# Performance work log

Measured on AMD Instinct MI355X. Metric: run time of the kernel, lower is better.

The kernel has to match this reference:

```python
import jax, jax.numpy as jnp
import numpy as np


def setup_inputs() -> dict:
    key = jax.random.key(0)
    ks = jax.random.split(key, 6)
    B, T, E, H, K = 4, 2048, 1024, 16, 3
    x = jax.random.normal(ks[0], (B, T, E), dtype=jnp.float32)
    mem_k = jax.random.normal(ks[1], (B, T, K, E), dtype=jnp.float32)
    mem_v = jax.random.normal(ks[2], (B, T, K, E), dtype=jnp.float32)
    W_attn = jax.random.normal(ks[3], (E, 3 * E), dtype=jnp.float32) * 0.02
    W_proj = jax.random.normal(ks[4], (E, E), dtype=jnp.float32) * 0.02
    gate_bias = jax.random.normal(ks[5], (H, 1, 1), dtype=jnp.float32)
    return {"x": x, "mem_k": mem_k, "mem_v": mem_v, "W_attn": W_attn,
            "W_proj": W_proj, "gate_bias": gate_bias}


def reference(x, mem_k, mem_v, W_attn, W_proj, gate_bias):
    B, T, E = x.shape
    H = gate_bias.shape[0]
    D = E // H
    K = mem_k.shape[2]
    # qkv projection (no bias)
    qkv = x @ W_attn                                   # [B,T,3E]
    q, k, v = jnp.split(qkv, 3, axis=-1)
    q = q.reshape(B, T, H, D).transpose(0, 2, 1, 3)    # [B,H,T,D]
    k = k.reshape(B, T, H, D).transpose(0, 2, 1, 3)
    v = v.reshape(B, T, H, D).transpose(0, 2, 1, 3)
    # causal SDPA (torch default scale = 1/sqrt(head_dim))
    scores = jnp.einsum('bhqd,bhkd->bhqk', q, k) / jnp.sqrt(jnp.asarray(D, q.dtype))
    causal = jnp.tril(jnp.ones((T, T), dtype=bool))
    scores = jnp.where(causal, scores, jnp.finfo(scores.dtype).min)
    attn = jax.nn.softmax(scores, axis=-1)
    y = jnp.einsum('bhqk,bhkd->bhqd', attn, v)         # [B,H,T,D]
    # top-k retrieved memory attention (k small, here 3)
    mk = mem_k.reshape(B, T, K, H, D).transpose(0, 3, 1, 2, 4)  # [B,H,T,K,D]
    mv = mem_v.reshape(B, T, K, H, D).transpose(0, 3, 1, 2, 4)
    # faithful to source: scale = n_embd / n_head**(-0.5) = E*sqrt(H)
    mem_scale = jnp.asarray(E, q.dtype) * jnp.sqrt(jnp.asarray(H, q.dtype))
    mem_qk = jnp.einsum('bhtd,bhtkd->bhtk', q, mk) * mem_scale
    mem_qk = jax.nn.softmax(mem_qk, axis=-1)
    mem_qkv = jnp.einsum('bhtk,bhtkd->bhtd', mem_qk, mv)  # [B,H,T,D]
    # gated fusion, gate_bias broadcasts [H,1,1] over [B,H,T,D]
    combined = mem_qkv * gate_bias + y * (1.0 - gate_bias)
    combined = combined.transpose(0, 2, 1, 3).reshape(B, T, E)
    out = combined @ W_proj
    return out
```

## Files before the change

kernel.cpp:

```cpp
#include <hip/hip_runtime.h>
#include <math.h>

#define Bsz 4
#define Tseq 2048
#define Ed 1024
#define Hh 16
#define E3 (3*Ed)
#define MROWS (Bsz*Tseq)

typedef short short8 __attribute__((ext_vector_type(8)));
typedef _Float16 half8 __attribute__((ext_vector_type(8)));
typedef float floatx4 __attribute__((ext_vector_type(4)));

__device__ __forceinline__ unsigned short f2bf(float f) {
  unsigned int u = __builtin_bit_cast(unsigned int, f);
  u += 0x7fffu + ((u >> 16) & 1u);
  return (unsigned short)(u >> 16);
}
__device__ __forceinline__ float bf2f(unsigned short u) {
  return __builtin_bit_cast(float, ((unsigned int)u) << 16);
}
__device__ __forceinline__ unsigned short f2h(float f) {
  _Float16 h = (_Float16)f;
  return __builtin_bit_cast(unsigned short, h);
}
__device__ __forceinline__ float h2f(unsigned short u) {
  return (float)__builtin_bit_cast(_Float16, u);
}
__device__ __forceinline__ int swz(int row, int col) {
  return row * 64 + ((((col >> 3) ^ (row & 7)) << 3) | (col & 7));
}
__device__ __forceinline__ void gload_lds16(const void* g, void* l) {
  __builtin_amdgcn_global_load_lds(
      (const __attribute__((address_space(1))) void*)g,
      (__attribute__((address_space(3))) void*)l, 16, 0, 0);
}

__global__ __launch_bounds__(256)
void cast_split_k(const float* __restrict__ s, unsigned short* __restrict__ bb,
                  unsigned short* __restrict__ hh, unsigned short* __restrict__ ll,
                  int n4) {
  int i = blockIdx.x * 256 + threadIdx.x;
  if (i >= n4) return;
  float4 v = ((const float4*)s)[i];
  float vv[4] = {v.x, v.y, v.z, v.w};
  unsigned short ob[4], oh[4], ol[4];
  #pragma unroll
  for (int j = 0; j < 4; ++j) {
    ob[j] = f2bf(vv[j]);
    unsigned short h = f2h(vv[j]);
    oh[j] = h;
    ol[j] = f2h(vv[j] - h2f(h));
  }
  ((uint2*)bb)[i] = *(uint2*)ob;
  ((uint2*)hh)[i] = *(uint2*)oh;
  ((uint2*)ll)[i] = *(uint2*)ol;
}

__global__ __launch_bounds__(256)
void transpose_cast(const float* __restrict__ src, int ld, int c0,
                    unsigned short* __restrict__ dst, int Krows) {
  __shared__ float t[64][65];
  const int kb = blockIdx.y * 64, nb = blockIdx.x * 64;
  const int tid = threadIdx.x;
  #pragma unroll
  for (int i = 0; i < 4; ++i) {
    int u = tid + i * 256;
    int r = u >> 4, c4 = u & 15;
    float4 v = *(const float4*)(src + (size_t)(kb + r) * ld + c0 + nb + c4 * 4);
    t[r][c4*4+0] = v.x; t[r][c4*4+1] = v.y; t[r][c4*4+2] = v.z; t[r][c4*4+3] = v.w;
  }
  __syncthreads();
  #pragma unroll
  for (int i = 0; i < 2; ++i) {
    int u = tid + i * 256;
    int rn = u >> 3, g = u & 7;
    unsigned short o[8];
    #pragma unroll
    for (int j = 0; j < 8; ++j) o[j] = f2bf(t[g*8+j][rn]);
    *(uint4*)(dst + (size_t)(nb + rn) * Krows + kb + g * 8) = *(uint4*)o;
  }
}

__global__ __launch_bounds__(256)
void transpose_split(const float* __restrict__ src, int ld, int c0,
                     unsigned short* __restrict__ dh, unsigned short* __restrict__ dl,
                     int Krows) {
  __shared__ float t[64][65];
  const int kb = blockIdx.y * 64, nb = blockIdx.x * 64;
  const int tid = threadIdx.x;
  #pragma unroll
  for (int i = 0; i < 4; ++i) {
    int u = tid + i * 256;
    int r = u >> 4, c4 = u & 15;
    float4 v = *(const float4*)(src + (size_t)(kb + r) * ld + c0 + nb + c4 * 4);
    t[r][c4*4+0] = v.x; t[r][c4*4+1] = v.y; t[r][c4*4+2] = v.z; t[r][c4*4+3] = v.w;
  }
  __syncthreads();
  #pragma unroll
  for (int i = 0; i < 2; ++i) {
    int u = tid + i * 256;
    int rn = u >> 3, g = u & 7;
    unsigned short oh[8], ol[8];
    #pragma unroll
    for (int j = 0; j < 8; ++j) {
      float f = t[g*8+j][rn];
      unsigned short h = f2h(f);
      oh[j] = h;
      ol[j] = f2h(f - h2f(h));
    }
    size_t off = (size_t)(nb + rn) * Krows + kb + g * 8;
    *(uint4*)(dh + off) = *(uint4*)oh;
    *(uint4*)(dl + off) = *(uint4*)ol;
  }
}

template<int N, int KD, bool OBF>
__global__ __launch_bounds__(256)
void gemm_bf16(const unsigned short* __restrict__ A,
               const unsigned short* __restrict__ Bt,
               void* __restrict__ C) {
  __shared__ __align__(16) unsigned short As[128 * 64];
  __shared__ __align__(16) unsigned short Bs[128 * 64];
  const int tid = threadIdx.x;
  const int w = tid >> 6, L = tid & 63, Ln = L & 15, Lq = L >> 4;
  const int wm = w & 1, wn = w >> 1;
  const int m0 = blockIdx.y * 128, n0 = blockIdx.x * 128;
  const int lr = L >> 3, lc = (L & 7) * 8;

  floatx4 acc[4][4];
  #pragma unroll
  for (int mt = 0; mt < 4; ++mt)
    #pragma unroll
    for (int nt = 0; nt < 4; ++nt) acc[mt][nt] = (floatx4)0.f;

  for (int kt = 0; kt < KD; kt += 64) {
    #pragma unroll
    for (int c = 0; c < 4; ++c) {
      int r0 = w * 32 + c * 8;
      gload_lds16(A  + (size_t)(m0 + r0 + lr) * KD + kt + lc, &As[r0 * 64]);
      gload_lds16(Bt + (size_t)(n0 + r0 + lr) * KD + kt + lc, &Bs[r0 * 64]);
    }
    __syncthreads();
    #pragma unroll
    for (int kc = 0; kc < 2; ++kc) {
      short8 af[4], bfr[4];
      #pragma unroll
      for (int mt = 0; mt < 4; ++mt)
        af[mt] = *(const short8*)&As[(wm*64 + mt*16 + Ln) * 64 + kc*32 + Lq*8];
      #pragma unroll
      for (int nt = 0; nt < 4; ++nt)
        bfr[nt] = *(const short8*)&Bs[(wn*64 + nt*16 + Ln) * 64 + kc*32 + Lq*8];
      #pragma unroll
      for (int mt = 0; mt < 4; ++mt)
        #pragma unroll
        for (int nt = 0; nt < 4; ++nt)
          acc[mt][nt] = __builtin_amdgcn_mfma_f32_16x16x32_bf16(af[mt], bfr[nt], acc[mt][nt], 0, 0, 0);
    }
    __syncthreads();
  }
  #pragma unroll
  for (int mt = 0; mt < 4; ++mt)
    #pragma unroll
    for (int nt = 0; nt < 4; ++nt)
      #pragma unroll
      for (int r = 0; r < 4; ++r) {
        size_t row = m0 + wm*64 + mt*16 + Lq*4 + r;
        int col = n0 + wn*64 + nt*16 + Ln;
        if (OBF) ((unsigned short*)C)[row * N + col] = f2bf(acc[mt][nt][r]);
        else     ((float*)C)[row * N + col] = acc[mt][nt][r];
      }
}

template<int N, int KD>
__global__ __launch_bounds__(256)
void gemm_f16x3(const unsigned short* __restrict__ Ah,
                const unsigned short* __restrict__ Al,
                const unsigned short* __restrict__ Bh,
                const unsigned short* __restrict__ Bl,
                float* __restrict__ C) {
  __shared__ __align__(16) unsigned short Ash[128 * 32];
  __shared__ __align__(16) unsigned short Asl[128 * 32];
  __shared__ __align__(16) unsigned short Bsh[128 * 32];
  __shared__ __align__(16) unsigned short Bsl[128 * 32];
  const int tid = threadIdx.x;
  const int w = tid >> 6, L = tid & 63, Ln = L & 15, Lq = L >> 4;
  const int wm = w & 1, wn = w >> 1;
  const int m0 = blockIdx.y * 128, n0 = blockIdx.x * 128;
  const int lr = L >> 2, lc = (L & 3) * 8;

  floatx4 acc[4][4];
  #pragma unroll
  for (int mt = 0; mt < 4; ++mt)
    #pragma unroll
    for (int nt = 0; nt < 4; ++nt) acc[mt][nt] = (floatx4)0.f;

  for (int kt = 0; kt < KD; kt += 32) {
    #pragma unroll
    for (int c = 0; c < 2; ++c) {
      int r0 = w * 32 + c * 16;
      size_t offA = (size_t)(m0 + r0 + lr) * KD + kt + lc;
      size_t offB = (size_t)(n0 + r0 + lr) * KD + kt + lc;
      gload_lds16(Ah + offA, &Ash[r0 * 32]);
      gload_lds16(Al + offA, &Asl[r0 * 32]);
      gload_lds16(Bh + offB, &Bsh[r0 * 32]);
      gload_lds16(Bl + offB, &Bsl[r0 * 32]);
    }
    __syncthreads();
    half8 afh[4], afl[4], bfh[4], bfl[4];
    #pragma unroll
    for (int mt = 0; mt < 4; ++mt) {
      afh[mt] = *(const half8*)&Ash[(wm*64 + mt*16 + Ln) * 32 + Lq*8];
      afl[mt] = *(const half8*)&Asl[(wm*64 + mt*16 + Ln) * 32 + Lq*8];
    }
    #pragma unroll
    for (int nt = 0; nt < 4; ++nt) {
      bfh[nt] = *(const half8*)&Bsh[(wn*64 + nt*16 + Ln) * 32 + Lq*8];
      bfl[nt] = *(const half8*)&Bsl[(wn*64 + nt*16 + Ln) * 32 + Lq*8];
    }
    #pragma unroll
    for (int mt = 0; mt < 4; ++mt)
      #pragma unroll
      for (int nt = 0; nt < 4; ++nt) {
        acc[mt][nt] = __builtin_amdgcn_mfma_f32_16x16x32_f16(afh[mt], bfh[nt], acc[mt][nt], 0, 0, 0);
        acc[mt][nt] = __builtin_amdgcn_mfma_f32_16x16x32_f16(afh[mt], bfl[nt], acc[mt][nt], 0, 0, 0);
        acc[mt][nt] = __builtin_amdgcn_mfma_f32_16x16x32_f16(afl[mt], bfh[nt], acc[mt][nt], 0, 0, 0);
      }
    __syncthreads();
  }
  #pragma unroll
  for (int mt = 0; mt < 4; ++mt)
    #pragma unroll
    for (int nt = 0; nt < 4; ++nt)
      #pragma unroll
      for (int r = 0; r < 4; ++r) {
        size_t row = m0 + wm*64 + mt*16 + Lq*4 + r;
        int col = n0 + wn*64 + nt*16 + Ln;
        C[row * N + col] = acc[mt][nt][r];
      }
}

__global__ __launch_bounds__(512, 4)
void flash_mfma(const float* __restrict__ qf, const unsigned short* __restrict__ kv,
                unsigned short* __restrict__ y) {
  __shared__ __align__(16) unsigned short Ks[2][64 * 64];
  __shared__ __align__(16) unsigned short Vt[2][64 * 64];
  __shared__ __align__(16) unsigned short Ps[8][16 * 64];
  const int ib = blockIdx.x;
  const int bh = blockIdx.y;
  const int b = bh >> 4, h = bh & 15;
  const int tid = threadIdx.x;
  const int w = tid >> 6, L = tid & 63;
  const int Ln = L & 15, Lq = L >> 4;
  const size_t base = (size_t)b * Tseq;
  const int hof = h * 64;

  for (int t = 0; t < 2; ++t) {
    const int qt = t ? ib : 15 - ib;
    const int q0 = qt * 128;
    const int nkt = 2 * qt + 2;

    short8 qfr[2];
    {
      const float* qp = qf + (base + q0 + w*16 + Ln) * Ed + hof;
      #pragma unroll
      for (int kc = 0; kc < 2; ++kc) {
        float v[8];
        *(float4*)&v[0] = *(const float4*)(qp + kc*32 + Lq*8);
        *(float4*)&v[4] = *(const float4*)(qp + kc*32 + Lq*8 + 4);
        short8 tt;
        #pragma unroll
        for (int j = 0; j < 8; ++j) tt[j] = (short)f2bf(v[j]);
        qfr[kc] = tt;
      }
    }

    float m_i[4], l_i[4];
    floatx4 O[4];
    #pragma unroll
    for (int r = 0; r < 4; ++r) { m_i[r] = -3.0e38f; l_i[r] = 0.f; }
    #pragma unroll
    for (int nt = 0; nt < 4; ++nt) O[nt] = (floatx4)0.f;

    {
      int c = tid >> 3, g = tid & 7;
      const unsigned short* kvp = kv + (base + c) * 2048 + hof + g * 8;
      uint4 k4 = *(const uint4*)kvp;
      *(uint4*)&Ks[0][c*64 + ((g ^ (c & 7)) << 3)] = k4;
      unsigned short vv[8];
      *(uint4*)vv = *(const uint4*)(kvp + 1024);
      #pragma unroll
      for (int j = 0; j < 8; ++j) Vt[0][swz(g*8 + j, c)] = vv[j];
    }
    __syncthreads();

    int cur = 0;
    for (int kt = 0; kt < nkt; ++kt) {
      uint4 kreg, vreg;
      const bool pre = (kt + 1 < nkt);
      const int c = tid >> 3, g = tid & 7;
      if (pre) {
        const unsigned short* kvp = kv + (base + (kt+1)*64 + c) * 2048 + hof + g * 8;
        kreg = *(const uint4*)kvp;
        vreg = *(const uint4*)(kvp + 1024);
      }

      short8 kb[4][2];
      #pragma unroll
      for (int nt = 0; nt < 4; ++nt) {
        int krow = nt*16 + Ln;
        #pragma unroll
        for (int kc = 0; kc < 2; ++kc)
          kb[nt][kc] = *(const short8*)&Ks[cur][krow*64 + ((((kc*4 + Lq) ^ (krow & 7)) << 3))];
      }
      floatx4 S[4];
      #pragma unroll
      for (int nt = 0; nt < 4; ++nt) {
        floatx4 a = (floatx4)0.f;
        a = __builtin_amdgcn_mfma_f32_16x16x32_bf16(qfr[0], kb[nt][0], a, 0, 0, 0);
        a = __builtin_amdgcn_mfma_f32_16x16x32_bf16(qfr[1], kb[nt][1], a, 0, 0, 0);
        S[nt] = a;
      }
      #pragma unroll
      for (int nt = 0; nt < 4; ++nt)
        #pragma unroll
        for (int r = 0; r < 4; ++r) S[nt][r] *= 0.125f;
      if (kt >= 2*qt) {
        int rowg = q0 + w*16 + Lq*4;
        #pragma unroll
        for (int nt = 0; nt < 4; ++nt) {
          int colg = kt*64 + nt*16 + Ln;
          #pragma unroll
          for (int r = 0; r < 4; ++r)
            if (colg > rowg + r) S[nt][r] = -3.0e38f;
        }
      }

      #pragma unroll
      for (int r = 0; r < 4; ++r) {
        float mx = fmaxf(fmaxf(S[0][r], S[1][r]), fmaxf(S[2][r], S[3][r]));
        mx = fmaxf(mx, __shfl_xor(mx, 1));
        mx = fmaxf(mx, __shfl_xor(mx, 2));
        mx = fmaxf(mx, __shfl_xor(mx, 4));
        mx = fmaxf(mx, __shfl_xor(mx, 8));
        float mnew = fmaxf(m_i[r], mx);
        float alpha = __expf(m_i[r] - mnew);
        m_i[r] = mnew;
        float rs = 0.f;
        #pragma unroll
        for (int nt = 0; nt < 4; ++nt) {
          float p = __expf(S[nt][r] - mnew);
          S[nt][r] = p;
          rs += p;
        }
        rs += __shfl_xor(rs, 1);
        rs += __shfl_xor(rs, 2);
        rs += __shfl_xor(rs, 4);
        rs += __shfl_xor(rs, 8);
        l_i[r] = l_i[r] * alpha + rs;
        #pragma unroll
        for (int nt = 0; nt < 4; ++nt) O[nt][r] *= alpha;
        int prow = Lq*4 + r;
        #pragma unroll
        for (int nt = 0; nt < 4; ++nt)
          Ps[w][swz(prow, nt*16 + Ln)] = f2bf(S[nt][r]);
      }

      short8 vb[4][2], pf[2];
      #pragma unroll
      for (int nt = 0; nt < 4; ++nt) {
        int vrow = nt*16 + Ln;
        #pragma unroll
        for (int kc = 0; kc < 2; ++kc)
          vb[nt][kc] = *(const short8*)&Vt[cur][vrow*64 + ((((kc*4 + Lq) ^ (vrow & 7)) << 3))];
      }
      {
        int prow = Ln;
        #pragma unroll
        for (int kc = 0; kc < 2; ++kc)
          pf[kc] = *(const short8*)&Ps[w][prow*64 + ((((kc*4 + Lq) ^ (prow & 7)) << 3))];
      }
      #pragma unroll
      for (int nt = 0; nt < 4; ++nt) {
        O[nt] = __builtin_amdgcn_mfma_f32_16x16x32_bf16(pf[0], vb[nt][0], O[nt], 0, 0, 0);
        O[nt] = __builtin_amdgcn_mfma_f32_16x16x32_bf16(pf[1], vb[nt][1], O[nt], 0, 0, 0);
      }

      if (pre) {
        *(uint4*)&Ks[cur^1][c*64 + ((g ^ (c & 7)) << 3)] = kreg;
        unsigned short vv[8];
        *(uint4*)vv = vreg;
        #pragma unroll
        for (int j = 0; j < 8; ++j) Vt[cur^1][swz(g*8 + j, c)] = vv[j];
      }
      __syncthreads();
      cur ^= 1;
    }

    #pragma unroll
    for (int r = 0; r < 4; ++r) {
      float inv = 1.f / l_i[r];
      size_t rb = (base + q0 + w*16 + Lq*4 + r) * Ed + hof;
      #pragma unroll
      for (int nt = 0; nt < 4; ++nt)
        y[rb + nt*16 + Ln] = f2bf(O[nt][r] * inv);
    }
  }
}

__global__ __launch_bounds__(256)
void mem_gate(const float* __restrict__ qf, const float* __restrict__ mem_k,
              const float* __restrict__ mem_v, const float* __restrict__ gate,
              unsigned short* __restrict__ y) {
  const int tid = threadIdx.x;
  const int lane = tid & 63;
  const int g = (blockIdx.x << 2) | (tid >> 6);
  const int h = g & 15;
  const int bt = g >> 4;
  const float q = qf[(size_t)bt * Ed + h*64 + lane];
  const size_t mb = ((size_t)bt * 3) * Ed + h*64 + lane;

  float s[3];
  #pragma unroll
  for (int k = 0; k < 3; ++k) {
    float p = q * mem_k[mb + (size_t)k * Ed];
    p += __shfl_xor(p, 1);  p += __shfl_xor(p, 2);  p += __shfl_xor(p, 4);
    p += __shfl_xor(p, 8);  p += __shfl_xor(p, 16); p += __shfl_xor(p, 32);
    s[k] = p * 4096.0f;
  }
  float mx = fmaxf(s[0], fmaxf(s[1], s[2]));
  float w0 = __expf(s[0] - mx), w1 = __expf(s[1] - mx), w2 = __expf(s[2] - mx);
  float inv = 1.f / (w0 + w1 + w2);
  float ov = (w0 * mem_v[mb] + w1 * mem_v[mb + Ed] + w2 * mem_v[mb + 2*Ed]) * inv;
  float gb = gate[h];
  unsigned short* yp = y + (size_t)bt * Ed + h*64 + lane;
  float yv = bf2f(*yp);
  *yp = f2bf(ov * gb + yv * (1.f - gb));
}

extern "C" void kernel_launch(void* const* d_in, const int* in_sizes, int n_in,
                              void* d_out, int out_size, void* d_ws, size_t ws_size,
                              hipStream_t stream) {
  const float* x      = (const float*)d_in[0];
  const float* mem_k  = (const float*)d_in[1];
  const float* mem_v  = (const float*)d_in[2];
  const float* W_attn = (const float*)d_in[3];
  const float* W_proj = (const float*)d_in[4];
  const float* gate   = (const float*)d_in[5];
  float* out = (float*)d_out;

  float* qf32          = (float*)d_ws;
  unsigned short* kvb  = (unsigned short*)(qf32 + (size_t)MROWS*Ed);
  unsigned short* ybf  = kvb + (size_t)MROWS*2048;
  unsigned short* xb   = ybf + (size_t)MROWS*Ed;
  unsigned short* wkv  = xb  + (size_t)MROWS*Ed;
  unsigned short* wp   = wkv + (size_t)2048*Ed;
  unsigned short* xh  = (unsigned short*)d_out;
  unsigned short* xl  = xh + (size_t)MROWS*Ed;
  unsigned short* wqh = kvb;
  unsigned short* wql = wqh + (size_t)Ed*Ed;

  cast_split_k<<<(MROWS*Ed/4 + 255)/256, 256, 0, stream>>>(x, xb, xh, xl, MROWS*Ed/4);
  transpose_split<<<dim3(Ed/64, Ed/64), 256, 0, stream>>>(W_attn, E3, 0, wqh, wql, Ed);
  transpose_cast<<<dim3(2048/64, Ed/64), 256, 0, stream>>>(W_attn, E3, Ed, wkv, Ed);
  transpose_cast<<<dim3(Ed/64, Ed/64), 256, 0, stream>>>(W_proj, Ed, 0, wp, Ed);
  gemm_f16x3<Ed, Ed>
      <<<dim3(Ed/128, MROWS/128), 256, 0, stream>>>(xh, xl, wqh, wql, qf32);
  gemm_bf16<2048, Ed, true>
      <<<dim3(2048/128, MROWS/128), 256, 0, stream>>>(xb, wkv, kvb);
  flash_mfma<<<dim3(8, Bsz*Hh), 512, 0, stream>>>(qf32, kvb, ybf);
  mem_gate<<<(MROWS*Hh)/4, 256, 0, stream>>>(qf32, mem_k, mem_v, gate, ybf);
  gemm_bf16<Ed, Ed, false>
      <<<dim3(Ed/128, MROWS/128), 256, 0, stream>>>(ybf, wp, out);
}
```

Baseline: 530.5 us.

## Fuse memory-gate into flash epilogue and deepen f16x3 GEMM K-tile

Removes the separate mem_gate kernel and computes the top-k memory attention and gated blend inside the flash attention epilogue. This avoids re-reading and re-writing the bf16 y buffer and saves one launch. The split-f16 GEMM now stages 64-wide K tiles per barrier instead of 32, which halves the number of sync rounds at the cost of doubled LDS use. The flash grid is also reordered so that heads vary fastest across blocks. The epilogue's memory loads are strided per lane and could underuse bandwidth compared with the old kernel's contiguous per-wave reads.

Result: slower. 559.8 us (+5.5%).

```diff
diff --git a/kernel.cpp b/kernel.cpp
--- a/kernel.cpp
+++ b/kernel.cpp
@@ -179,15 +179,15 @@
                 const unsigned short* __restrict__ Bh,
                 const unsigned short* __restrict__ Bl,
                 float* __restrict__ C) {
-  __shared__ __align__(16) unsigned short Ash[128 * 32];
-  __shared__ __align__(16) unsigned short Asl[128 * 32];
-  __shared__ __align__(16) unsigned short Bsh[128 * 32];
-  __shared__ __align__(16) unsigned short Bsl[128 * 32];
+  __shared__ __align__(16) unsigned short Ash[128 * 64];
+  __shared__ __align__(16) unsigned short Asl[128 * 64];
+  __shared__ __align__(16) unsigned short Bsh[128 * 64];
+  __shared__ __align__(16) unsigned short Bsl[128 * 64];
   const int tid = threadIdx.x;
   const int w = tid >> 6, L = tid & 63, Ln = L & 15, Lq = L >> 4;
   const int wm = w & 1, wn = w >> 1;
   const int m0 = blockIdx.y * 128, n0 = blockIdx.x * 128;
-  const int lr = L >> 2, lc = (L & 3) * 8;
+  const int lr = L >> 3, lc = (L & 7) * 8;
 
   floatx4 acc[4][4];
   #pragma unroll
@@ -195,37 +195,40 @@
     #pragma unroll
     for (int nt = 0; nt < 4; ++nt) acc[mt][nt] = (floatx4)0.f;
 
-  for (int kt = 0; kt < KD; kt += 32) {
-    #pragma unroll
-    for (int c = 0; c < 2; ++c) {
-      int r0 = w * 32 + c * 16;
+  for (int kt = 0; kt < KD; kt += 64) {
+    #pragma unroll
+    for (int c = 0; c < 4; ++c) {
+      int r0 = w * 32 + c * 8;
       size_t offA = (size_t)(m0 + r0 + lr) * KD + kt + lc;
       size_t offB = (size_t)(n0 + r0 + lr) * KD + kt + lc;
-      gload_lds16(Ah + offA, &Ash[r0 * 32]);
-      gload_lds16(Al + offA, &Asl[r0 * 32]);
-      gload_lds16(Bh + offB, &Bsh[r0 * 32]);
-      gload_lds16(Bl + offB, &Bsl[r0 * 32]);
+      gload_lds16(Ah + offA, &Ash[r0 * 64]);
+      gload_lds16(Al + offA, &Asl[r0 * 64]);
+      gload_lds16(Bh + offB, &Bsh[r0 * 64]);
+      gload_lds16(Bl + offB, &Bsl[r0 * 64]);
     }
     __syncthreads();
-    half8 afh[4], afl[4], bfh[4], bfl[4];
-    #pragma unroll
-    for (int mt = 0; mt < 4; ++mt) {
-      afh[mt] = *(const half8*)&Ash[(wm*64 + mt*16 + Ln) * 32 + Lq*8];
-      afl[mt] = *(const half8*)&Asl[(wm*64 + mt*16 + Ln) * 32 + Lq*8];
-    }
-    #pragma unroll
-    for (int nt = 0; nt < 4; ++nt) {
-      bfh[nt] = *(const half8*)&Bsh[(wn*64 + nt*16 + Ln) * 32 + Lq*8];
-      bfl[nt] = *(const half8*)&Bsl[(wn*64 + nt*16 + Ln) * 32 + Lq*8];
-    }
-    #pragma unroll
-    for (int mt = 0; mt < 4; ++mt)
-      #pragma unroll
-      for (int nt = 0; nt < 4; ++nt) {
-        acc[mt][nt] = __builtin_amdgcn_mfma_f32_16x16x32_f16(afh[mt], bfh[nt], acc[mt][nt], 0, 0, 0);
-        acc[mt][nt] = __builtin_amdgcn_mfma_f32_16x16x32_f16(afh[mt], bfl[nt], acc[mt][nt], 0, 0, 0);
-        acc[mt][nt] = __builtin_amdgcn_mfma_f32_16x16x32_f16(afl[mt], bfh[nt], acc[mt][nt], 0, 0, 0);
-      }
+    #pragma unroll
+    for (int kc = 0; kc < 2; ++kc) {
+      half8 afh[4], afl[4], bfh[4], bfl[4];
+      #pragma unroll
+      for (int mt = 0; mt < 4; ++mt) {
+        afh[mt] = *(const half8*)&Ash[(wm*64 + mt*16 + Ln) * 64 + kc*32 + Lq*8];
+        afl[mt] = *(const half8*)&Asl[(wm*64 + mt*16 + Ln) * 64 + kc*32 + Lq*8];
+      }
+      #pragma unroll
+      for (int nt = 0; nt < 4; ++nt) {
+        bfh[nt] = *(const half8*)&Bsh[(wn*64 + nt*16 + Ln) * 64 + kc*32 + Lq*8];
+        bfl[nt] = *(const half8*)&Bsl[(wn*64 + nt*16 + Ln) * 64 + kc*32 + Lq*8];
+      }
+      #pragma unroll
+      for (int mt = 0; mt < 4; ++mt)
+        #pragma unroll
+        for (int nt = 0; nt < 4; ++nt) {
+          acc[mt][nt] = __builtin_amdgcn_mfma_f32_16x16x32_f16(afh[mt], bfh[nt], acc[mt][nt], 0, 0, 0);
+          acc[mt][nt] = __builtin_amdgcn_mfma_f32_16x16x32_f16(afh[mt], bfl[nt], acc[mt][nt], 0, 0, 0);
+          acc[mt][nt] = __builtin_amdgcn_mfma_f32_16x16x32_f16(afl[mt], bfh[nt], acc[mt][nt], 0, 0, 0);
+        }
+    }
     __syncthreads();
   }
   #pragma unroll
@@ -242,18 +245,20 @@
 
 __global__ __launch_bounds__(512, 4)
 void flash_mfma(const float* __restrict__ qf, const unsigned short* __restrict__ kv,
-                unsigned short* __restrict__ y) {
+                const float* __restrict__ mem_k, const float* __restrict__ mem_v,
+                const float* __restrict__ gate, unsigned short* __restrict__ y) {
   __shared__ __align__(16) unsigned short Ks[2][64 * 64];
   __shared__ __align__(16) unsigned short Vt[2][64 * 64];
   __shared__ __align__(16) unsigned short Ps[8][16 * 64];
-  const int ib = blockIdx.x;
-  const int bh = blockIdx.y;
+  const int bh = blockIdx.x;
+  const int ib = blockIdx.y;
   const int b = bh >> 4, h = bh & 15;
   const int tid = threadIdx.x;
   const int w = tid >> 6, L = tid & 63;
   const int Ln = L & 15, Lq = L >> 4;
   const size_t base = (size_t)b * Tseq;
   const int hof = h * 64;
+  const float gb = gate[h];
 
   for (int t = 0; t < 2; ++t) {
     const int qt = t ? ib : 15 - ib;
@@ -399,43 +404,41 @@
 
     #pragma unroll
     for (int r = 0; r < 4; ++r) {
-      float inv = 1.f / l_i[r];
-      size_t rb = (base + q0 + w*16 + Lq*4 + r) * Ed + hof;
-      #pragma unroll
-      for (int nt = 0; nt < 4; ++nt)
-        y[rb + nt*16 + Ln] = f2bf(O[nt][r] * inv);
-    }
-  }
-}
-
-__global__ __launch_bounds__(256)
-void mem_gate(const float* __restrict__ qf, const float* __restrict__ mem_k,
-              const float* __restrict__ mem_v, const float* __restrict__ gate,
-              unsigned short* __restrict__ y) {
-  const int tid = threadIdx.x;
-  const int lane = tid & 63;
-  const int g = (blockIdx.x << 2) | (tid >> 6);
-  const int h = g & 15;
-  const int bt = g >> 4;
-  const float q = qf[(size_t)bt * Ed + h*64 + lane];
-  const size_t mb = ((size_t)bt * 3) * Ed + h*64 + lane;
-
-  float s[3];
-  #pragma unroll
-  for (int k = 0; k < 3; ++k) {
-    float p = q * mem_k[mb + (size_t)k * Ed];
-    p += __shfl_xor(p, 1);  p += __shfl_xor(p, 2);  p += __shfl_xor(p, 4);
-    p += __shfl_xor(p, 8);  p += __shfl_xor(p, 16); p += __shfl_xor(p, 32);
-    s[k] = p * 4096.0f;
-  }
-  float mx = fmaxf(s[0], fmaxf(s[1], s[2]));
-  float w0 = __expf(s[0] - mx), w1 = __expf(s[1] - mx), w2 = __expf(s[2] - mx);
-  float inv = 1.f / (w0 + w1 + w2);
-  float ov = (w0 * mem_v[mb] + w1 * mem_v[mb + Ed] + w2 * mem_v[mb + 2*Ed]) * inv;
-  float gb = gate[h];
-  unsigned short* yp = y + (size_t)bt * Ed + h*64 + lane;
-  float yv = bf2f(*yp);
-  *yp = f2bf(ov * gb + yv * (1.f - gb));
+      const int row = q0 + w*16 + Lq*4 + r;
+      const size_t grow = base + row;
+      const float inv = 1.f / l_i[r];
+      float qv[4];
+      const float* qp = qf + grow * Ed + hof;
+      #pragma unroll
+      for (int nt = 0; nt < 4; ++nt) qv[nt] = qp[nt*16 + Ln];
+      const float* mkp = mem_k + (grow * 3) * Ed + hof;
+      const float* mvp = mem_v + (grow * 3) * Ed + hof;
+      float s[3];
+      #pragma unroll
+      for (int k = 0; k < 3; ++k) {
+        float p = 0.f;
+        #pragma unroll
+        for (int nt = 0; nt < 4; ++nt)
+          p += qv[nt] * mkp[(size_t)k * Ed + nt*16 + Ln];
+        p += __shfl_xor(p, 1);
+        p += __shfl_xor(p, 2);
+        p += __shfl_xor(p, 4);
+        p += __shfl_xor(p, 8);
+        s[k] = p * 4096.0f;
+      }
+      float mx = fmaxf(s[0], fmaxf(s[1], s[2]));
+      float w0 = __expf(s[0] - mx), w1 = __expf(s[1] - mx), w2 = __expf(s[2] - mx);
+      float winv = 1.f / (w0 + w1 + w2);
+      size_t rb = grow * Ed + hof;
+      #pragma unroll
+      for (int nt = 0; nt < 4; ++nt) {
+        int cc = nt*16 + Ln;
+        float ov = (w0 * mvp[cc] + w1 * mvp[Ed + cc] + w2 * mvp[2*Ed + cc]) * winv;
+        float yv = O[nt][r] * inv;
+        y[rb + cc] = f2bf(ov * gb + yv * (1.f - gb));
+      }
+    }
+  }
 }
 
 extern "C" void kernel_launch(void* const* d_in, const int* in_sizes, int n_in,
@@ -468,8 +471,7 @@
       <<<dim3(Ed/128, MROWS/128), 256, 0, stream>>>(xh, xl, wqh, wql, qf32);
   gemm_bf16<2048, Ed, true>
       <<<dim3(2048/128, MROWS/128), 256, 0, stream>>>(xb, wkv, kvb);
-  flash_mfma<<<dim3(8, Bsz*Hh), 512, 0, stream>>>(qf32, kvb, ybf);
-  mem_gate<<<(MROWS*Hh)/4, 256, 0, stream>>>(qf32, mem_k, mem_v, gate, ybf);
+  flash_mfma<<<dim3(Bsz*Hh, 8), 512, 0, stream>>>(qf32, kvb, mem_k, mem_v, gate, ybf);
   gemm_bf16<Ed, Ed, false>
       <<<dim3(Ed/128, MROWS/128), 256, 0, stream>>>(ybf, wp, out);
 }
```

## Double K-tile depth in f16x3 GEMM and use 128-key tiles in flash attention

Applied to the files above, without the earlier changes.

The split-f16 GEMM now stages 64-wide K slices per iteration instead of 32, which halves the number of barrier-separated load phases. The flash attention kernel processes 128 keys per iteration instead of 64, halving its loop trips and barriers, and folds the 1/sqrt(D) scale into the bf16 conversion of Q. The P·V product is done in two 64-column halves so the per-warp P staging buffer stays the same size. In exchange, LDS use roughly doubles in both kernels, which may lower occupancy, and the diagonal block now wastes more masked work.

Result: slower. 649.7 us (+22.5%).

```diff
diff --git a/kernel.cpp b/kernel.cpp
--- a/kernel.cpp
+++ b/kernel.cpp
@@ -29,6 +29,9 @@
 }
 __device__ __forceinline__ int swz(int row, int col) {
   return row * 64 + ((((col >> 3) ^ (row & 7)) << 3) | (col & 7));
+}
+__device__ __forceinline__ int swz128(int row, int col) {
+  return row * 128 + ((((col >> 3) ^ (row & 7)) << 3) | (col & 7));
 }
 __device__ __forceinline__ void gload_lds16(const void* g, void* l) {
   __builtin_amdgcn_global_load_lds(
@@ -179,15 +182,15 @@
                 const unsigned short* __restrict__ Bh,
                 const unsigned short* __restrict__ Bl,
                 float* __restrict__ C) {
-  __shared__ __align__(16) unsigned short Ash[128 * 32];
-  __shared__ __align__(16) unsigned short Asl[128 * 32];
-  __shared__ __align__(16) unsigned short Bsh[128 * 32];
-  __shared__ __align__(16) unsigned short Bsl[128 * 32];
+  __shared__ __align__(16) unsigned short Ash[128 * 64];
+  __shared__ __align__(16) unsigned short Asl[128 * 64];
+  __shared__ __align__(16) unsigned short Bsh[128 * 64];
+  __shared__ __align__(16) unsigned short Bsl[128 * 64];
   const int tid = threadIdx.x;
   const int w = tid >> 6, L = tid & 63, Ln = L & 15, Lq = L >> 4;
   const int wm = w & 1, wn = w >> 1;
   const int m0 = blockIdx.y * 128, n0 = blockIdx.x * 128;
-  const int lr = L >> 2, lc = (L & 3) * 8;
+  const int lr = L >> 3, lc = (L & 7) * 8;
 
   floatx4 acc[4][4];
   #pragma unroll
@@ -195,37 +198,40 @@
     #pragma unroll
     for (int nt = 0; nt < 4; ++nt) acc[mt][nt] = (floatx4)0.f;
 
-  for (int kt = 0; kt < KD; kt += 32) {
-    #pragma unroll
-    for (int c = 0; c < 2; ++c) {
-      int r0 = w * 32 + c * 16;
+  for (int kt = 0; kt < KD; kt += 64) {
+    #pragma unroll
+    for (int c = 0; c < 4; ++c) {
+      int r0 = w * 32 + c * 8;
       size_t offA = (size_t)(m0 + r0 + lr) * KD + kt + lc;
       size_t offB = (size_t)(n0 + r0 + lr) * KD + kt + lc;
-      gload_lds16(Ah + offA, &Ash[r0 * 32]);
-      gload_lds16(Al + offA, &Asl[r0 * 32]);
-      gload_lds16(Bh + offB, &Bsh[r0 * 32]);
-      gload_lds16(Bl + offB, &Bsl[r0 * 32]);
+      gload_lds16(Ah + offA, &Ash[r0 * 64]);
+      gload_lds16(Al + offA, &Asl[r0 * 64]);
+      gload_lds16(Bh + offB, &Bsh[r0 * 64]);
+      gload_lds16(Bl + offB, &Bsl[r0 * 64]);
     }
     __syncthreads();
-    half8 afh[4], afl[4], bfh[4], bfl[4];
-    #pragma unroll
-    for (int mt = 0; mt < 4; ++mt) {
-      afh[mt] = *(const half8*)&Ash[(wm*64 + mt*16 + Ln) * 32 + Lq*8];
-      afl[mt] = *(const half8*)&Asl[(wm*64 + mt*16 + Ln) * 32 + Lq*8];
-    }
-    #pragma unroll
-    for (int nt = 0; nt < 4; ++nt) {
-      bfh[nt] = *(const half8*)&Bsh[(wn*64 + nt*16 + Ln) * 32 + Lq*8];
-      bfl[nt] = *(const half8*)&Bsl[(wn*64 + nt*16 + Ln) * 32 + Lq*8];
-    }
-    #pragma unroll
-    for (int mt = 0; mt < 4; ++mt)
+    #pragma unroll
+    for (int kc = 0; kc < 2; ++kc) {
+      half8 afh[4], afl[4], bfh[4], bfl[4];
+      #pragma unroll
+      for (int mt = 0; mt < 4; ++mt) {
+        afh[mt] = *(const half8*)&Ash[(wm*64 + mt*16 + Ln) * 64 + kc*32 + Lq*8];
+        afl[mt] = *(const half8*)&Asl[(wm*64 + mt*16 + Ln) * 64 + kc*32 + Lq*8];
+      }
       #pragma unroll
       for (int nt = 0; nt < 4; ++nt) {
-        acc[mt][nt] = __builtin_amdgcn_mfma_f32_16x16x32_f16(afh[mt], bfh[nt], acc[mt][nt], 0, 0, 0);
-        acc[mt][nt] = __builtin_amdgcn_mfma_f32_16x16x32_f16(afh[mt], bfl[nt], acc[mt][nt], 0, 0, 0);
-        acc[mt][nt] = __builtin_amdgcn_mfma_f32_16x16x32_f16(afl[mt], bfh[nt], acc[mt][nt], 0, 0, 0);
-      }
+        bfh[nt] = *(const half8*)&Bsh[(wn*64 + nt*16 + Ln) * 64 + kc*32 + Lq*8];
+        bfl[nt] = *(const half8*)&Bsl[(wn*64 + nt*16 + Ln) * 64 + kc*32 + Lq*8];
+      }
+      #pragma unroll
+      for (int mt = 0; mt < 4; ++mt)
+        #pragma unroll
+        for (int nt = 0; nt < 4; ++nt) {
+          acc[mt][nt] = __builtin_amdgcn_mfma_f32_16x16x32_f16(afh[mt], bfh[nt], acc[mt][nt], 0, 0, 0);
+          acc[mt][nt] = __builtin_amdgcn_mfma_f32_16x16x32_f16(afh[mt], bfl[nt], acc[mt][nt], 0, 0, 0);
+          acc[mt][nt] = __builtin_amdgcn_mfma_f32_16x16x32_f16(afl[mt], bfh[nt], acc[mt][nt], 0, 0, 0);
+        }
+    }
     __syncthreads();
   }
   #pragma unroll
@@ -243,8 +249,8 @@
 __global__ __launch_bounds__(512, 4)
 void flash_mfma(const float* __restrict__ qf, const unsigned short* __restrict__ kv,
                 unsigned short* __restrict__ y) {
-  __shared__ __align__(16) unsigned short Ks[2][64 * 64];
-  __shared__ __align__(16) unsigned short Vt[2][64 * 64];
+  __shared__ __align__(16) unsigned short Ks[2][128 * 64];
+  __shared__ __align__(16) unsigned short Vt[2][64 * 128];
   __shared__ __align__(16) unsigned short Ps[8][16 * 64];
   const int ib = blockIdx.x;
   const int bh = blockIdx.y;
@@ -258,7 +264,7 @@
   for (int t = 0; t < 2; ++t) {
     const int qt = t ? ib : 15 - ib;
     const int q0 = qt * 128;
-    const int nkt = 2 * qt + 2;
+    const int nkt = qt + 1;
 
     short8 qfr[2];
     {
@@ -270,7 +276,7 @@
         *(float4*)&v[4] = *(const float4*)(qp + kc*32 + Lq*8 + 4);
         short8 tt;
         #pragma unroll
-        for (int j = 0; j < 8; ++j) tt[j] = (short)f2bf(v[j]);
+        for (int j = 0; j < 8; ++j) tt[j] = (short)f2bf(v[j] * 0.125f);
         qfr[kc] = tt;
       }
     }
@@ -282,54 +288,52 @@
     #pragma unroll
     for (int nt = 0; nt < 4; ++nt) O[nt] = (floatx4)0.f;
 
-    {
-      int c = tid >> 3, g = tid & 7;
+    #pragma unroll
+    for (int i = 0; i < 2; ++i) {
+      int u = tid + i * 512;
+      int c = u >> 3, g = u & 7;
       const unsigned short* kvp = kv + (base + c) * 2048 + hof + g * 8;
       uint4 k4 = *(const uint4*)kvp;
       *(uint4*)&Ks[0][c*64 + ((g ^ (c & 7)) << 3)] = k4;
       unsigned short vv[8];
       *(uint4*)vv = *(const uint4*)(kvp + 1024);
       #pragma unroll
-      for (int j = 0; j < 8; ++j) Vt[0][swz(g*8 + j, c)] = vv[j];
+      for (int j = 0; j < 8; ++j) Vt[0][swz128(g*8 + j, c)] = vv[j];
     }
     __syncthreads();
 
     int cur = 0;
     for (int kt = 0; kt < nkt; ++kt) {
-      uint4 kreg, vreg;
+      uint4 kreg[2], vreg[2];
       const bool pre = (kt + 1 < nkt);
-      const int c = tid >> 3, g = tid & 7;
       if (pre) {
-        const unsigned short* kvp = kv + (base + (kt+1)*64 + c) * 2048 + hof + g * 8;
-        kreg = *(const uint4*)kvp;
-        vreg = *(const uint4*)(kvp + 1024);
-      }
-
-      short8 kb[4][2];
-      #pragma unroll
-      for (int nt = 0; nt < 4; ++nt) {
+        #pragma unroll
+        for (int i = 0; i < 2; ++i) {
+          int u = tid + i * 512;
+          int c = u >> 3, g = u & 7;
+          const unsigned short* kvp =
+              kv + (base + (kt+1)*128 + c) * 2048 + hof + g * 8;
+          kreg[i] = *(const uint4*)kvp;
+          vreg[i] = *(const uint4*)(kvp + 1024);
+        }
+      }
+
+      floatx4 S[8];
+      #pragma unroll
+      for (int nt = 0; nt < 8; ++nt) {
         int krow = nt*16 + Ln;
-        #pragma unroll
-        for (int kc = 0; kc < 2; ++kc)
-          kb[nt][kc] = *(const short8*)&Ks[cur][krow*64 + ((((kc*4 + Lq) ^ (krow & 7)) << 3))];
-      }
-      floatx4 S[4];
-      #pragma unroll
-      for (int nt = 0; nt < 4; ++nt) {
+        short8 kb0 = *(const short8*)&Ks[cur][krow*64 + (((Lq ^ (krow & 7)) << 3))];
+        short8 kb1 = *(const short8*)&Ks[cur][krow*64 + ((((4 + Lq) ^ (krow & 7)) << 3))];
         floatx4 a = (floatx4)0.f;
-        a = __builtin_amdgcn_mfma_f32_16x16x32_bf16(qfr[0], kb[nt][0], a, 0, 0, 0);
-        a = __builtin_amdgcn_mfma_f32_16x16x32_bf16(qfr[1], kb[nt][1], a, 0, 0, 0);
+        a = __builtin_amdgcn_mfma_f32_16x16x32_bf16(qfr[0], kb0, a, 0, 0, 0);
+        a = __builtin_amdgcn_mfma_f32_16x16x32_bf16(qfr[1], kb1, a, 0, 0, 0);
         S[nt] = a;
       }
-      #pragma unroll
-      for (int nt = 0; nt < 4; ++nt)
-        #pragma unroll
-        for (int r = 0; r < 4; ++r) S[nt][r] *= 0.125f;
-      if (kt >= 2*qt) {
+      if (kt == qt) {
         int rowg = q0 + w*16 + Lq*4;
         #pragma unroll
-        for (int nt = 0; nt < 4; ++nt) {
-          int colg = kt*64 + nt*16 + Ln;
+        for (int nt = 0; nt < 8; ++nt) {
+          int colg = kt*128 + nt*16 + Ln;
           #pragma unroll
           for (int r = 0; r < 4; ++r)
             if (colg > rowg + r) S[nt][r] = -3.0e38f;
@@ -338,7 +342,9 @@
 
       #pragma unroll
       for (int r = 0; r < 4; ++r) {
-        float mx = fmaxf(fmaxf(S[0][r], S[1][r]), fmaxf(S[2][r], S[3][r]));
+        float mx = S[0][r];
+        #pragma unroll
+        for (int nt = 1; nt < 8; ++nt) mx = fmaxf(mx, S[nt][r]);
         mx = fmaxf(mx, __shfl_xor(mx, 1));
         mx = fmaxf(mx, __shfl_xor(mx, 2));
         mx = fmaxf(mx, __shfl_xor(mx, 4));
@@ -348,7 +354,7 @@
         m_i[r] = mnew;
         float rs = 0.f;
         #pragma unroll
-        for (int nt = 0; nt < 4; ++nt) {
+        for (int nt = 0; nt < 8; ++nt) {
           float p = __expf(S[nt][r] - mnew);
           S[nt][r] = p;
           rs += p;
@@ -366,32 +372,53 @@
           Ps[w][swz(prow, nt*16 + Ln)] = f2bf(S[nt][r]);
       }
 
-      short8 vb[4][2], pf[2];
-      #pragma unroll
-      for (int nt = 0; nt < 4; ++nt) {
-        int vrow = nt*16 + Ln;
+      {
+        short8 pf[2];
         #pragma unroll
         for (int kc = 0; kc < 2; ++kc)
-          vb[nt][kc] = *(const short8*)&Vt[cur][vrow*64 + ((((kc*4 + Lq) ^ (vrow & 7)) << 3))];
+          pf[kc] = *(const short8*)&Ps[w][Ln*64 + ((((kc*4 + Lq) ^ (Ln & 7)) << 3))];
+        #pragma unroll
+        for (int nt = 0; nt < 4; ++nt) {
+          int vrow = nt*16 + Ln;
+          short8 vb0 = *(const short8*)&Vt[cur][vrow*128 + (((Lq ^ (vrow & 7)) << 3))];
+          short8 vb1 = *(const short8*)&Vt[cur][vrow*128 + ((((4 + Lq) ^ (vrow & 7)) << 3))];
+          O[nt] = __builtin_amdgcn_mfma_f32_16x16x32_bf16(pf[0], vb0, O[nt], 0, 0, 0);
+          O[nt] = __builtin_amdgcn_mfma_f32_16x16x32_bf16(pf[1], vb1, O[nt], 0, 0, 0);
+        }
+      }
+      #pragma unroll
+      for (int r = 0; r < 4; ++r) {
+        int prow = Lq*4 + r;
+        #pragma unroll
+        for (int nt = 4; nt < 8; ++nt)
+          Ps[w][swz(prow, (nt-4)*16 + Ln)] = f2bf(S[nt][r]);
       }
       {
-        int prow = Ln;
+        short8 pf[2];
         #pragma unroll
         for (int kc = 0; kc < 2; ++kc)
-          pf[kc] = *(const short8*)&Ps[w][prow*64 + ((((kc*4 + Lq) ^ (prow & 7)) << 3))];
-      }
-      #pragma unroll
-      for (int nt = 0; nt < 4; ++nt) {
-        O[nt] = __builtin_amdgcn_mfma_f32_16x16x32_bf16(pf[0], vb[nt][0], O[nt], 0, 0, 0);
-        O[nt] = __builtin_amdgcn_mfma_f32_16x16x32_bf16(pf[1], vb[nt][1], O[nt], 0, 0, 0);
+          pf[kc] = *(const short8*)&Ps[w][Ln*64 + ((((kc*4 + Lq) ^ (Ln & 7)) << 3))];
+        #pragma unroll
+        for (int nt = 0; nt < 4; ++nt) {
+          int vrow = nt*16 + Ln;
+          short8 vb2 = *(const short8*)&Vt[cur][vrow*128 + ((((8 + Lq) ^ (vrow & 7)) << 3))];
+          short8 vb3 = *(const short8*)&Vt[cur][vrow*128 + ((((12 + Lq) ^ (vrow & 7)) << 3))];
+          O[nt] = __builtin_amdgcn_mfma_f32_16x16x32_bf16(pf[0], vb2, O[nt], 0, 0, 0);
+          O[nt] = __builtin_amdgcn_mfma_f32_16x16x32_bf16(pf[1], vb3, O[nt], 0, 0, 0);
+        }
       }
 
       if (pre) {
-        *(uint4*)&Ks[cur^1][c*64 + ((g ^ (c & 7)) << 3)] = kreg;
-        unsigned short vv[8];
-        *(uint4*)vv = vreg;
-        #pragma unroll
-        for (int j = 0; j < 8; ++j) Vt[cur^1][swz(g*8 + j, c)] = vv[j];
+        #pragma unroll
+        for (int i = 0; i < 2; ++i) {
+          int u = tid + i * 512;
+          int c = u >> 3, g = u & 7;
+          *(uint4*)&Ks[cur^1][c*64 + ((g ^ (c & 7)) << 3)] = kreg[i];
+          unsigned short vv[8];
+          *(uint4*)vv = vreg[i];
+          #pragma unroll
+          for (int j = 0; j < 8; ++j) Vt[cur^1][swz128(g*8 + j, c)] = vv[j];
+        }
       }
       __syncthreads();
       cur ^= 1;
```
